# Optimization experiments

Hardware: AMD Instinct MI355X
Metric: run time of the kernel (lower is better)

## Reference

```python
import jax, jax.numpy as jnp
import numpy as np

D_MODEL = 1024
NUM_HEADS = 16
HEAD_DIM = D_MODEL // NUM_HEADS
HIDDEN = 4096
EPS = 1e-10


def _layernorm(x, gamma, beta):
    mean = jnp.mean(x, axis=-1, keepdims=True)
    var = jnp.var(x, axis=-1, keepdims=True)  # unbiased=False
    return gamma * (x - mean) / jnp.sqrt(var + EPS) + beta


def setup_inputs() -> dict:
    key = jax.random.key(0)
    ks = jax.random.split(key, 16)
    s = 0.02
    d, h = D_MODEL, HIDDEN
    inp = {
        "x": jax.random.normal(ks[0], (4, 2048, d), dtype=jnp.float32),
        "Wq": jax.random.normal(ks[1], (d, d), dtype=jnp.float32) * s,
        "bq": jnp.zeros((d,), jnp.float32),
        "Wk": jax.random.normal(ks[2], (d, d), dtype=jnp.float32) * s,
        "bk": jnp.zeros((d,), jnp.float32),
        "Wv": jax.random.normal(ks[3], (d, d), dtype=jnp.float32) * s,
        "bv": jnp.zeros((d,), jnp.float32),
        "Wo": jax.random.normal(ks[4], (d, d), dtype=jnp.float32) * s,
        "bo": jnp.zeros((d,), jnp.float32),
        "W1": jax.random.normal(ks[5], (d, h), dtype=jnp.float32) * s,
        "b1": jnp.zeros((h,), jnp.float32),
        "W2": jax.random.normal(ks[6], (h, d), dtype=jnp.float32) * s,
        "b2": jnp.zeros((d,), jnp.float32),
        "gamma1": jnp.ones((d,), jnp.float32),
        "beta1": jnp.zeros((d,), jnp.float32),
        "gamma2": jnp.ones((d,), jnp.float32),
        "beta2": jnp.zeros((d,), jnp.float32),
    }
    return inp


def reference(x, Wq, bq, Wk, bk, Wv, bv, Wo, bo, W1, b1, W2, b2,
              gamma1, beta1, gamma2, beta2):
    B, S, D = x.shape
    H, hd = NUM_HEADS, HEAD_DIM
    scale = jnp.sqrt(jnp.float32(hd))

    # --- sublayer 1: self-attention on norm(x), residual add ---
    xn = _layernorm(x, gamma1, beta1)
    Q = (xn @ Wq + bq).reshape(B, S, H, hd).transpose(0, 2, 1, 3)  # [B,H,S,hd]
    K = (xn @ Wk + bk).reshape(B, S, H, hd).transpose(0, 2, 1, 3)
    V = (xn @ Wv + bv).reshape(B, S, H, hd).transpose(0, 2, 1, 3)
    scores = jnp.einsum("bhqd,bhkd->bhqk", Q, K) / scale  # [B,H,S,S]
    attn = jax.nn.softmax(scores, axis=-1)
    ctx = jnp.einsum("bhqk,bhkd->bhqd", attn, V)  # [B,H,S,hd]
    ctx = ctx.transpose(0, 2, 1, 3).reshape(B, S, D)
    x = x + (ctx @ Wo + bo)

    # --- sublayer 2: FFN on norm(x), residual add ---
    xn = _layernorm(x, gamma2, beta2)
    h = jax.nn.gelu(xn @ W1 + b1, approximate=False)  # torch F.gelu default = erf
    x = x + (h @ W2 + b2)
    return x
```

## Files before the change

kernel.cpp:

```cpp
#include <hip/hip_runtime.h>
#include <stdint.h>

#define D_MODEL 1024
#define HIDDEN  4096
#define SEQ     2048
#define NTOK    8192
#define NHEAD   16
#define HDIM    64

typedef unsigned short u16;
typedef __attribute__((ext_vector_type(8))) __bf16 bf16x8;
typedef __attribute__((ext_vector_type(4))) float f32x4;

__device__ __forceinline__ u16 f2bf(float f) {
  union { float f; unsigned u; } c; c.f = f;
  unsigned u = c.u + 0x7fffu + ((c.u >> 16) & 1u);
  return (u16)(u >> 16);
}

__device__ __forceinline__ void gload16(const void* g, void* l) {
  __builtin_amdgcn_global_load_lds((const __attribute__((address_space(1))) void*)g,
                                   (__attribute__((address_space(3))) void*)l, 16, 0, 0);
}

__global__ void transpose_cvt4(const float* __restrict__ A0, const float* __restrict__ A1,
                               const float* __restrict__ A2, const float* __restrict__ A3,
                               u16* __restrict__ O) {
  __shared__ float t[32][33];
  const int z = blockIdx.z;
  const float* W = (z == 0) ? A0 : (z == 1) ? A1 : (z == 2) ? A2 : A3;
  u16* Wt = O + ((size_t)z << 20);
  const int k0 = blockIdx.y * 32, n0 = blockIdx.x * 32;
  const int tx = threadIdx.x, ty = threadIdx.y;
#pragma unroll
  for (int p = 0; p < 4; ++p)
    t[ty + p * 8][tx] = W[(size_t)(k0 + ty + p * 8) * D_MODEL + n0 + tx];
  __syncthreads();
#pragma unroll
  for (int p = 0; p < 4; ++p) {
    const int n = ty + p * 8;
    Wt[(size_t)(n0 + n) * D_MODEL + k0 + tx] = f2bf(t[tx][n]);
  }
}

__global__ void transpose_cvt(const float* __restrict__ W, u16* __restrict__ Wt, int K, int N) {
  __shared__ float t[32][33];
  const int k0 = blockIdx.y * 32, n0 = blockIdx.x * 32;
  const int tx = threadIdx.x, ty = threadIdx.y;
#pragma unroll
  for (int p = 0; p < 4; ++p)
    t[ty + p * 8][tx] = W[(size_t)(k0 + ty + p * 8) * N + n0 + tx];
  __syncthreads();
#pragma unroll
  for (int p = 0; p < 4; ++p) {
    const int n = ty + p * 8;
    Wt[(size_t)(n0 + n) * K + k0 + tx] = f2bf(t[tx][n]);
  }
}

__global__ __launch_bounds__(256)
void ln_kernel(const float* __restrict__ x, const float* __restrict__ gamma,
               const float* __restrict__ beta, u16* __restrict__ out) {
  const int row = blockIdx.x;
  const int tid = threadIdx.x;
  const float4 v = ((const float4*)(x + (size_t)row * D_MODEL))[tid];
  float s = v.x + v.y + v.z + v.w;
  float q = v.x * v.x + v.y * v.y + v.z * v.z + v.w * v.w;
#pragma unroll
  for (int o = 32; o > 0; o >>= 1) { s += __shfl_down(s, o); q += __shfl_down(q, o); }
  __shared__ float ps[4], pq[4];
  const int wid = tid >> 6, lane = tid & 63;
  if (lane == 0) { ps[wid] = s; pq[wid] = q; }
  __syncthreads();
  s = ps[0] + ps[1] + ps[2] + ps[3];
  q = pq[0] + pq[1] + pq[2] + pq[3];
  const float mean = s * (1.0f / D_MODEL);
  const float var = q * (1.0f / D_MODEL) - mean * mean;
  const float rstd = rsqrtf(var + 1e-10f);
  const float4 gv = ((const float4*)gamma)[tid];
  const float4 bv = ((const float4*)beta)[tid];
  ushort4 o4;
  o4.x = f2bf((v.x - mean) * rstd * gv.x + bv.x);
  o4.y = f2bf((v.y - mean) * rstd * gv.y + bv.y);
  o4.z = f2bf((v.z - mean) * rstd * gv.z + bv.z);
  o4.w = f2bf((v.w - mean) * rstd * gv.w + bv.w);
  ((ushort4*)(out + (size_t)row * D_MODEL))[tid] = o4;
}

#define SLOT_AE (256 * 32)
#define SLOT_BE (128 * 32)
#define SLOT_E  (SLOT_AE + SLOT_BE)
#define SLOT_BYTES (SLOT_E * 2)

template <int EPI, int KPY, int KPX>
__global__ __launch_bounds__(512, 4)
void gemm32(const u16* __restrict__ A, const u16* __restrict__ Bt,
            const float* __restrict__ bias, const float* __restrict__ bias2,
            const float* __restrict__ res, void* __restrict__ outp, void* __restrict__ outp2,
            int M, int N, int K) {
  __shared__ u16 Ls[3 * SLOT_E];
  const int tid = threadIdx.x;
  const int wid = tid >> 6, lane = tid & 63;
  const int g = lane >> 4, lr = lane & 15;
  const int wr = wid >> 1, wc = wid & 1;

  const int xcd = blockIdx.x & 7, l = blockIdx.x >> 3;
  int bx, by;
  if (KPY > 0) { by = xcd * KPY + (l % KPY); bx = l / KPY; }
  else         { bx = xcd * KPX + (l % KPX); by = l / KPX; }
  const int m0 = by * 256, n0 = bx * 128;

  const int NT = K >> 5;

  const int rA0 = tid >> 2, cc0 = ((tid & 3) ^ (rA0 & 3)) << 3;
  const int u1 = tid + 512;
  const int rA1 = u1 >> 2, cc1 = (((u1 & 3) ^ (rA1 & 3))) << 3;
  const u16* pA0 = A + (size_t)(m0 + rA0) * K + cc0;
  const u16* pA1 = A + (size_t)(m0 + rA1) * K + cc1;
  const u16* pB0 = Bt + (size_t)(n0 + rA0) * K + cc0;
  const int dA0 = wid * 1024;
  const int dA1 = wid * 1024 + 8192;
  const int dB0 = SLOT_AE * 2 + wid * 1024;

  auto stage = [&](int slot) {
    char* sb = (char*)Ls + slot * SLOT_BYTES;
    gload16(pA0, sb + dA0);
    gload16(pA1, sb + dA1);
    gload16(pB0, sb + dB0);
    pA0 += 32; pA1 += 32; pB0 += 32;
  };

  stage(0); stage(1); stage(2);

  f32x4 acc[4][4] = {};
  const int cx = (g ^ (lr & 3)) << 3;

  for (int t = 0; t < NT; ++t) {
    if (t + 3 <= NT)      asm volatile("s_waitcnt vmcnt(6)" ::: "memory");
    else if (t + 2 <= NT) asm volatile("s_waitcnt vmcnt(3)" ::: "memory");
    else                  asm volatile("s_waitcnt vmcnt(0)" ::: "memory");
    asm volatile("s_barrier" ::: "memory");

    const int slot = t % 3;
    const u16* sA = Ls + slot * SLOT_E;
    const u16* sB = sA + SLOT_AE;
    bf16x8 af[4], bfr[4];
#pragma unroll
    for (int mf = 0; mf < 4; ++mf)
      af[mf] = *(const bf16x8*)(sA + (wr * 64 + mf * 16 + lr) * 32 + cx);
#pragma unroll
    for (int nf = 0; nf < 4; ++nf)
      bfr[nf] = *(const bf16x8*)(sB + (wc * 64 + nf * 16 + lr) * 32 + cx);

    __builtin_amdgcn_s_setprio(1);
#pragma unroll
    for (int mf = 0; mf < 4; ++mf)
#pragma unroll
      for (int nf = 0; nf < 4; ++nf)
        acc[mf][nf] = __builtin_amdgcn_mfma_f32_16x16x32_bf16(af[mf], bfr[nf], acc[mf][nf], 0, 0, 0);
    __builtin_amdgcn_s_setprio(0);

    if (t + 3 < NT) {
      asm volatile("s_barrier" ::: "memory");
      stage(slot);
    }
  }

#pragma unroll
  for (int mf = 0; mf < 4; ++mf)
#pragma unroll
    for (int nf = 0; nf < 4; ++nf) {
      const int gn = n0 + wc * 64 + nf * 16 + lr;
      const int gm = m0 + wr * 64 + mf * 16 + 4 * g;
#pragma unroll
      for (int r = 0; r < 4; ++r) {
        const float av = acc[mf][nf][r];
        if (EPI == 0) {
          ((u16*)outp)[(size_t)(gm + r) * N + gn] = f2bf(av + bias[gn]);
        } else if (EPI == 1) {
          const size_t idx = (size_t)(gm + r) * N + gn;
          ((float*)outp)[idx] = av + bias[gn] + res[idx];
        } else if (EPI == 2) {
          const float v = av + bias[gn];
          ((u16*)outp)[(size_t)(gm + r) * N + gn] =
              f2bf(0.5f * v * (1.0f + erff(v * 0.7071067811865475f)));
        } else if (EPI == 3) {
          const int gn_p = (gn & ~63) | ((gn & 15) << 2) | ((gn >> 4) & 3);
          ((u16*)outp)[(size_t)(gm + r) * N + gn_p] = f2bf(av + bias[gm + r]);
        } else {
          const int side = gn >> 10, col = gn & 1023;
          u16* o = (u16*)(side ? outp2 : outp);
          float t_ = av + (side ? bias2[col] : bias[col]);
          if (!side) t_ *= 0.18033688011112042f;
          o[(size_t)(gm + r) * 1024 + col] = f2bf(t_);
        }
      }
    }
}

__global__ __launch_bounds__(256, 4)
void attn_kernel(const u16* __restrict__ Q, const u16* __restrict__ K,
                 const u16* __restrict__ Vt, u16* __restrict__ ctxo) {
  const int L = blockIdx.x;
  const int q0 = ((L >> 3) & 15) * 128;
  const int bh = ((L >> 7) << 3) | (L & 7);
  const int b = bh >> 4, h = bh & 15;
  const int tid = threadIdx.x, wid = tid >> 6, lane = tid & 63;
  const int g = lane >> 4, lr = lane & 15;
  const size_t base = ((size_t)b * SEQ) * D_MODEL + h * HDIM;
  const size_t vbase = ((size_t)h * HDIM) * NTOK + (size_t)b * SEQ;

#define AST 76
  __shared__ u16 Ks[64 * AST];
  __shared__ u16 Vts[64 * AST];
  __shared__ u16 Ps[128 * AST];

  const int qw = wid * 32;

#pragma unroll
  for (int i = 0; i < 4; ++i) {
    const int ch = tid + 256 * i, row = ch >> 3, j = ch & 7;
    *(bf16x8*)(Ps + row * AST + j * 8) =
        *(const bf16x8*)(Q + base + (size_t)(q0 + row) * D_MODEL + j * 8);
  }
  __syncthreads();
  bf16x8 aq[2][2];
#pragma unroll
  for (int qf = 0; qf < 2; ++qf)
#pragma unroll
    for (int ks = 0; ks < 2; ++ks)
      aq[qf][ks] = *(const bf16x8*)(Ps + (qw + qf * 16 + lr) * AST + ks * 32 + g * 8);

  f32x4 o[2][4] = {};
  float lrun[2][4] = {};

  for (int kv0 = 0; kv0 < SEQ; kv0 += 64) {
    __syncthreads();
#pragma unroll
    for (int i = 0; i < 2; ++i) {
      const int row = (tid >> 3) + i * 32, j = tid & 7;
      *(bf16x8*)(Ks + row * AST + j * 8) =
          *(const bf16x8*)(K + base + (size_t)(kv0 + row) * D_MODEL + j * 8);
      *(bf16x8*)(Vts + row * AST + j * 8) =
          *(const bf16x8*)(Vt + vbase + (size_t)row * NTOK + kv0 + j * 8);
    }
    __syncthreads();

    f32x4 s[2][4] = {};
    __builtin_amdgcn_s_setprio(1);
#pragma unroll
    for (int ks = 0; ks < 2; ++ks)
#pragma unroll
      for (int kf = 0; kf < 4; ++kf) {
        const bf16x8 bk = *(const bf16x8*)(Ks + (kf * 16 + lr) * AST + ks * 32 + g * 8);
#pragma unroll
        for (int qf = 0; qf < 2; ++qf)
          s[qf][kf] = __builtin_amdgcn_mfma_f32_16x16x32_bf16(aq[qf][ks], bk, s[qf][kf], 0, 0, 0);
      }
    __builtin_amdgcn_s_setprio(0);

#pragma unroll
    for (int qf = 0; qf < 2; ++qf)
#pragma unroll
      for (int r = 0; r < 4; ++r) {
        float p0, p1, p2, p3;
        asm("v_exp_f32 %0, %1" : "=v"(p0) : "v"(s[qf][0][r]));
        asm("v_exp_f32 %0, %1" : "=v"(p1) : "v"(s[qf][1][r]));
        asm("v_exp_f32 %0, %1" : "=v"(p2) : "v"(s[qf][2][r]));
        asm("v_exp_f32 %0, %1" : "=v"(p3) : "v"(s[qf][3][r]));
        lrun[qf][r] += (p0 + p1) + (p2 + p3);
        unsigned lo, hi;
        asm("v_cvt_pk_bf16_f32 %0, %1, %2" : "=v"(lo) : "v"(p0), "v"(p1));
        asm("v_cvt_pk_bf16_f32 %0, %1, %2" : "=v"(hi) : "v"(p2), "v"(p3));
        *(uint2*)(Ps + (qw + qf * 16 + 4 * g + r) * AST + lr * 4) = make_uint2(lo, hi);
      }
    asm volatile("s_waitcnt lgkmcnt(0)" ::: "memory");

    __builtin_amdgcn_s_setprio(1);
#pragma unroll
    for (int ks = 0; ks < 2; ++ks) {
      bf16x8 pf[2];
#pragma unroll
      for (int qf = 0; qf < 2; ++qf)
        pf[qf] = *(const bf16x8*)(Ps + (qw + qf * 16 + lr) * AST + ks * 32 + g * 8);
#pragma unroll
      for (int df = 0; df < 4; ++df) {
        const bf16x8 vf = *(const bf16x8*)(Vts + (df * 16 + lr) * AST + ks * 32 + g * 8);
#pragma unroll
        for (int qf = 0; qf < 2; ++qf)
          o[qf][df] = __builtin_amdgcn_mfma_f32_16x16x32_bf16(pf[qf], vf, o[qf][df], 0, 0, 0);
      }
    }
    __builtin_amdgcn_s_setprio(0);
  }

#pragma unroll
  for (int off = 1; off < 16; off <<= 1)
#pragma unroll
    for (int qf = 0; qf < 2; ++qf)
#pragma unroll
      for (int r = 0; r < 4; ++r)
        lrun[qf][r] += __shfl_xor(lrun[qf][r], off);

#pragma unroll
  for (int qf = 0; qf < 2; ++qf)
#pragma unroll
    for (int r = 0; r < 4; ++r) {
      const float rinv = 1.0f / lrun[qf][r];
      const int qrow = q0 + qw + qf * 16 + 4 * g + r;
#pragma unroll
      for (int df = 0; df < 4; ++df)
        ctxo[base + (size_t)qrow * D_MODEL + df * 16 + lr] = f2bf(o[qf][df][r] * rinv);
    }
#undef AST
}

extern "C" void kernel_launch(void* const* d_in, const int* in_sizes, int n_in,
                              void* d_out, int out_size, void* d_ws, size_t ws_size,
                              hipStream_t stream) {
  const float* x  = (const float*)d_in[0];
  const float* Wq = (const float*)d_in[1];
  const float* bq = (const float*)d_in[2];
  const float* Wk = (const float*)d_in[3];
  const float* bk = (const float*)d_in[4];
  const float* Wv = (const float*)d_in[5];
  const float* bv = (const float*)d_in[6];
  const float* Wo = (const float*)d_in[7];
  const float* bo = (const float*)d_in[8];
  const float* W1 = (const float*)d_in[9];
  const float* b1 = (const float*)d_in[10];
  const float* W2 = (const float*)d_in[11];
  const float* b2 = (const float*)d_in[12];
  const float* gamma1 = (const float*)d_in[13];
  const float* beta1  = (const float*)d_in[14];
  const float* gamma2 = (const float*)d_in[15];
  const float* beta2  = (const float*)d_in[16];
  float* out = (float*)d_out;

  const size_t M1 = 1u << 20;
  u16* w   = (u16*)d_ws;
  u16* WtQ = w;
  u16* WtV = w + 2 * M1;
  u16* WtO = w + 3 * M1;
  u16* Wt1 = w + 4 * M1;
  u16* Wt2 = w + 8 * M1;
  u16* xn  = w + 12 * M1;
  u16* Qb  = w + 20 * M1;
  u16* Kb  = w + 28 * M1;
  u16* Vtb = w + 36 * M1;
  u16* ctx = w + 44 * M1;
  u16* hb  = w + 20 * M1;
  float* x1 = (float*)(w + 52 * M1);

  const dim3 tb(32, 8);
  transpose_cvt4<<<dim3(32, 32, 4), tb, 0, stream>>>(Wq, Wk, Wv, Wo, WtQ);
  transpose_cvt<<<dim3(HIDDEN / 32, D_MODEL / 32), tb, 0, stream>>>(W1, Wt1, D_MODEL, HIDDEN);
  transpose_cvt<<<dim3(D_MODEL / 32, HIDDEN / 32), tb, 0, stream>>>(W2, Wt2, HIDDEN, D_MODEL);

  ln_kernel<<<NTOK, 256, 0, stream>>>(x, gamma1, beta1, xn);

  gemm32<6, 4, 0><<<512, 512, 0, stream>>>(xn, WtQ, bq, bk, nullptr, Qb, Kb,
                                           NTOK, 2048, D_MODEL);
  gemm32<3, 0, 8><<<256, 512, 0, stream>>>(WtV, xn, bv, nullptr, nullptr, Vtb, nullptr,
                                           D_MODEL, NTOK, D_MODEL);

  attn_kernel<<<1024, 256, 0, stream>>>(Qb, Kb, Vtb, ctx);

  gemm32<1, 4, 0><<<256, 512, 0, stream>>>(ctx, WtO, bo, nullptr, x, x1, nullptr,
                                           NTOK, D_MODEL, D_MODEL);

  ln_kernel<<<NTOK, 256, 0, stream>>>(x1, gamma2, beta2, xn);

  gemm32<2, 4, 0><<<1024, 512, 0, stream>>>(xn, Wt1, b1, nullptr, nullptr, hb, nullptr,
                                            NTOK, HIDDEN, D_MODEL);
  gemm32<1, 4, 0><<<256, 512, 0, stream>>>(hb, Wt2, b2, nullptr, x1, out, nullptr,
                                           NTOK, D_MODEL, HIDDEN);
}
```

Baseline: 384.6 us.

## Replace triple-buffered 256x128 GEMM with single-buffered 128x128 tile kernel

Replaces the 512-thread GEMM, which used a 256x128 tile and a three-slot async LDS pipeline with vmcnt-based waits, with a 256-thread 128x128 tile kernel. The new kernel uses a single LDS buffer with two barriers per K-step and no prefetch overlap. Grid sizes and block-swizzle parameters are adjusted to match. This doubles the block count and shrinks LDS use per block, but global loads are no longer overlapped with MFMA work, and A/B reuse per tile drops.

```diff
diff --git a/kernel.cpp b/kernel.cpp
--- a/kernel.cpp
+++ b/kernel.cpp
@@ -87,71 +87,53 @@
   ((ushort4*)(out + (size_t)row * D_MODEL))[tid] = o4;
 }
 
-#define SLOT_AE (256 * 32)
-#define SLOT_BE (128 * 32)
-#define SLOT_E  (SLOT_AE + SLOT_BE)
-#define SLOT_BYTES (SLOT_E * 2)
-
 template <int EPI, int KPY, int KPX>
-__global__ __launch_bounds__(512, 4)
-void gemm32(const u16* __restrict__ A, const u16* __restrict__ Bt,
+__global__ __launch_bounds__(256, 3)
+void gemm97(const u16* __restrict__ A, const u16* __restrict__ Bt,
             const float* __restrict__ bias, const float* __restrict__ bias2,
             const float* __restrict__ res, void* __restrict__ outp, void* __restrict__ outp2,
             int M, int N, int K) {
-  __shared__ u16 Ls[3 * SLOT_E];
+  __shared__ u16 As[128 * 32];
+  __shared__ u16 Bs[128 * 32];
   const int tid = threadIdx.x;
   const int wid = tid >> 6, lane = tid & 63;
   const int g = lane >> 4, lr = lane & 15;
-  const int wr = wid >> 1, wc = wid & 1;
+  const int wm = (wid & 1) << 6, wn = (wid >> 1) << 6;
 
   const int xcd = blockIdx.x & 7, l = blockIdx.x >> 3;
   int bx, by;
   if (KPY > 0) { by = xcd * KPY + (l % KPY); bx = l / KPY; }
   else         { bx = xcd * KPX + (l % KPX); by = l / KPX; }
-  const int m0 = by * 256, n0 = bx * 128;
+  const int m0 = by * 128, n0 = bx * 128;
 
   const int NT = K >> 5;
 
-  const int rA0 = tid >> 2, cc0 = ((tid & 3) ^ (rA0 & 3)) << 3;
-  const int u1 = tid + 512;
-  const int rA1 = u1 >> 2, cc1 = (((u1 & 3) ^ (rA1 & 3))) << 3;
-  const u16* pA0 = A + (size_t)(m0 + rA0) * K + cc0;
-  const u16* pA1 = A + (size_t)(m0 + rA1) * K + cc1;
-  const u16* pB0 = Bt + (size_t)(n0 + rA0) * K + cc0;
-  const int dA0 = wid * 1024;
-  const int dA1 = wid * 1024 + 8192;
-  const int dB0 = SLOT_AE * 2 + wid * 1024;
-
-  auto stage = [&](int slot) {
-    char* sb = (char*)Ls + slot * SLOT_BYTES;
-    gload16(pA0, sb + dA0);
-    gload16(pA1, sb + dA1);
-    gload16(pB0, sb + dB0);
-    pA0 += 32; pA1 += 32; pB0 += 32;
-  };
-
-  stage(0); stage(1); stage(2);
+  const int r0 = tid >> 2;
+  const int c0 = ((tid & 3) ^ (r0 & 3)) << 3;
+  const u16* pA0 = A + (size_t)(m0 + r0) * K + c0;
+  const u16* pA1 = A + (size_t)(m0 + r0 + 64) * K + c0;
+  const u16* pB0 = Bt + (size_t)(n0 + r0) * K + c0;
+  const u16* pB1 = Bt + (size_t)(n0 + r0 + 64) * K + c0;
+  const int d0 = (tid & 192) * 16;
 
   f32x4 acc[4][4] = {};
   const int cx = (g ^ (lr & 3)) << 3;
 
   for (int t = 0; t < NT; ++t) {
-    if (t + 3 <= NT)      asm volatile("s_waitcnt vmcnt(6)" ::: "memory");
-    else if (t + 2 <= NT) asm volatile("s_waitcnt vmcnt(3)" ::: "memory");
-    else                  asm volatile("s_waitcnt vmcnt(0)" ::: "memory");
-    asm volatile("s_barrier" ::: "memory");
-
-    const int slot = t % 3;
-    const u16* sA = Ls + slot * SLOT_E;
-    const u16* sB = sA + SLOT_AE;
+    __syncthreads();
+    gload16(pA0, (char*)As + d0);
+    gload16(pA1, (char*)As + d0 + 4096);
+    gload16(pB0, (char*)Bs + d0);
+    gload16(pB1, (char*)Bs + d0 + 4096);
+    pA0 += 32; pA1 += 32; pB0 += 32; pB1 += 32;
+    __syncthreads();
+
     bf16x8 af[4], bfr[4];
 #pragma unroll
-    for (int mf = 0; mf < 4; ++mf)
-      af[mf] = *(const bf16x8*)(sA + (wr * 64 + mf * 16 + lr) * 32 + cx);
-#pragma unroll
-    for (int nf = 0; nf < 4; ++nf)
-      bfr[nf] = *(const bf16x8*)(sB + (wc * 64 + nf * 16 + lr) * 32 + cx);
-
+    for (int f = 0; f < 4; ++f) {
+      af[f] = *(const bf16x8*)(As + (wm + f * 16 + lr) * 32 + cx);
+      bfr[f] = *(const bf16x8*)(Bs + (wn + f * 16 + lr) * 32 + cx);
+    }
     __builtin_amdgcn_s_setprio(1);
 #pragma unroll
     for (int mf = 0; mf < 4; ++mf)
@@ -159,19 +141,14 @@
       for (int nf = 0; nf < 4; ++nf)
         acc[mf][nf] = __builtin_amdgcn_mfma_f32_16x16x32_bf16(af[mf], bfr[nf], acc[mf][nf], 0, 0, 0);
     __builtin_amdgcn_s_setprio(0);
-
-    if (t + 3 < NT) {
-      asm volatile("s_barrier" ::: "memory");
-      stage(slot);
-    }
   }
 
 #pragma unroll
   for (int mf = 0; mf < 4; ++mf)
 #pragma unroll
     for (int nf = 0; nf < 4; ++nf) {
-      const int gn = n0 + wc * 64 + nf * 16 + lr;
-      const int gm = m0 + wr * 64 + mf * 16 + 4 * g;
+      const int gn = n0 + wn + nf * 16 + lr;
+      const int gm = m0 + wm + mf * 16 + 4 * g;
 #pragma unroll
       for (int r = 0; r < 4; ++r) {
         const float av = acc[mf][nf][r];
@@ -359,20 +336,20 @@
 
   ln_kernel<<<NTOK, 256, 0, stream>>>(x, gamma1, beta1, xn);
 
-  gemm32<6, 4, 0><<<512, 512, 0, stream>>>(xn, WtQ, bq, bk, nullptr, Qb, Kb,
-                                           NTOK, 2048, D_MODEL);
-  gemm32<3, 0, 8><<<256, 512, 0, stream>>>(WtV, xn, bv, nullptr, nullptr, Vtb, nullptr,
+  gemm97<6, 8, 0><<<1024, 256, 0, stream>>>(xn, WtQ, bq, bk, nullptr, Qb, Kb,
+                                            NTOK, 2048, D_MODEL);
+  gemm97<3, 1, 0><<<512, 256, 0, stream>>>(WtV, xn, bv, nullptr, nullptr, Vtb, nullptr,
                                            D_MODEL, NTOK, D_MODEL);
 
   attn_kernel<<<1024, 256, 0, stream>>>(Qb, Kb, Vtb, ctx);
 
-  gemm32<1, 4, 0><<<256, 512, 0, stream>>>(ctx, WtO, bo, nullptr, x, x1, nullptr,
+  gemm97<1, 8, 0><<<512, 256, 0, stream>>>(ctx, WtO, bo, nullptr, x, x1, nullptr,
                                            NTOK, D_MODEL, D_MODEL);
 
   ln_kernel<<<NTOK, 256, 0, stream>>>(x1, gamma2, beta2, xn);
 
-  gemm32<2, 4, 0><<<1024, 512, 0, stream>>>(xn, Wt1, b1, nullptr, nullptr, hb, nullptr,
+  gemm97<2, 8, 0><<<2048, 256, 0, stream>>>(xn, Wt1, b1, nullptr, nullptr, hb, nullptr,
                                             NTOK, HIDDEN, D_MODEL);
-  gemm32<1, 4, 0><<<256, 512, 0, stream>>>(hb, Wt2, b2, nullptr, x1, out, nullptr,
+  gemm97<1, 8, 0><<<512, 256, 0, stream>>>(hb, Wt2, b2, nullptr, x1, out, nullptr,
                                            NTOK, D_MODEL, HIDDEN);
 }
```

After: 398.7 us. 3.7% more time.

## Add 128x128-tile GEMM with 64-wide K steps for FFN layers

Applied to the files above, without the earlier changes.

Adds a new gemm64 kernel that uses 128x128 output tiles, 256 threads, 64-element K slices with XOR-swizzled LDS, and 4x4 MFMA fragments per wave. The two FFN GEMMs now use it in place of the prior gemm32 kernel, with more, smaller blocks and a different XCD mapping. The aim is to raise block-level parallelism and occupancy and cut per-iteration sync overhead by doing more MFMA work per barrier. The loop is single-buffered with two barriers per K step, so memory latency may not be hidden as well as in the old kernel.

```diff
diff --git a/kernel.cpp b/kernel.cpp
--- a/kernel.cpp
+++ b/kernel.cpp
@@ -198,6 +198,104 @@
     }
 }
 
+template <int EPI, int KPY, int KPX>
+__global__ __launch_bounds__(256, 3)
+void gemm64(const u16* __restrict__ A, const u16* __restrict__ Bt,
+            const float* __restrict__ bias, const float* __restrict__ bias2,
+            const float* __restrict__ res, void* __restrict__ outp, void* __restrict__ outp2,
+            int M, int N, int K) {
+  __shared__ u16 As[128 * 64];
+  __shared__ u16 Bs[128 * 64];
+  const int tid = threadIdx.x;
+  const int wid = tid >> 6, lane = tid & 63;
+  const int g = lane >> 4, lr = lane & 15;
+  const int wm = (wid & 1) << 6, wn = (wid >> 1) << 6;
+
+  const int xcd = blockIdx.x & 7, l = blockIdx.x >> 3;
+  int bx, by;
+  if (KPY > 0) { by = xcd * KPY + (l % KPY); bx = l / KPY; }
+  else         { bx = xcd * KPX + (l % KPX); by = l / KPX; }
+  const int m0 = by * 128, n0 = bx * 128;
+
+  const int NT = K >> 6;
+
+  const int r0 = tid >> 3;
+  const int csw = ((tid & 7) ^ (r0 & 7)) << 3;
+  const u16* pA[4];
+  const u16* pB[4];
+#pragma unroll
+  for (int i = 0; i < 4; ++i) {
+    pA[i] = A + (size_t)(m0 + r0 + i * 32) * K + csw;
+    pB[i] = Bt + (size_t)(n0 + r0 + i * 32) * K + csw;
+  }
+  const int db = (tid & 192) * 16;
+
+  f32x4 acc[4][4] = {};
+
+  for (int t = 0; t < NT; ++t) {
+    __syncthreads();
+#pragma unroll
+    for (int i = 0; i < 4; ++i) {
+      gload16(pA[i], (char*)As + db + i * 4096);
+      gload16(pB[i], (char*)Bs + db + i * 4096);
+      pA[i] += 64; pB[i] += 64;
+    }
+    __syncthreads();
+
+#pragma unroll
+    for (int ks = 0; ks < 2; ++ks) {
+      bf16x8 af[4], bfr[4];
+#pragma unroll
+      for (int f = 0; f < 4; ++f) {
+        const int ra = wm + f * 16 + lr;
+        const int rb = wn + f * 16 + lr;
+        const int co = ((ks * 4 + g) ^ (lr & 7)) * 8;
+        af[f] = *(const bf16x8*)(As + ra * 64 + co);
+        bfr[f] = *(const bf16x8*)(Bs + rb * 64 + co);
+      }
+      __builtin_amdgcn_s_setprio(1);
+#pragma unroll
+      for (int mf = 0; mf < 4; ++mf)
+#pragma unroll
+        for (int nf = 0; nf < 4; ++nf)
+          acc[mf][nf] =
+              __builtin_amdgcn_mfma_f32_16x16x32_bf16(af[mf], bfr[nf], acc[mf][nf], 0, 0, 0);
+      __builtin_amdgcn_s_setprio(0);
+    }
+  }
+
+#pragma unroll
+  for (int mf = 0; mf < 4; ++mf)
+#pragma unroll
+    for (int nf = 0; nf < 4; ++nf) {
+      const int gn = n0 + wn + nf * 16 + lr;
+      const int gm = m0 + wm + mf * 16 + 4 * g;
+#pragma unroll
+      for (int r = 0; r < 4; ++r) {
+        const float av = acc[mf][nf][r];
+        if (EPI == 0) {
+          ((u16*)outp)[(size_t)(gm + r) * N + gn] = f2bf(av + bias[gn]);
+        } else if (EPI == 1) {
+          const size_t idx = (size_t)(gm + r) * N + gn;
+          ((float*)outp)[idx] = av + bias[gn] + res[idx];
+        } else if (EPI == 2) {
+          const float v = av + bias[gn];
+          ((u16*)outp)[(size_t)(gm + r) * N + gn] =
+              f2bf(0.5f * v * (1.0f + erff(v * 0.7071067811865475f)));
+        } else if (EPI == 3) {
+          const int gn_p = (gn & ~63) | ((gn & 15) << 2) | ((gn >> 4) & 3);
+          ((u16*)outp)[(size_t)(gm + r) * N + gn_p] = f2bf(av + bias[gm + r]);
+        } else {
+          const int side = gn >> 10, col = gn & 1023;
+          u16* o = (u16*)(side ? outp2 : outp);
+          float t_ = av + (side ? bias2[col] : bias[col]);
+          if (!side) t_ *= 0.18033688011112042f;
+          o[(size_t)(gm + r) * 1024 + col] = f2bf(t_);
+        }
+      }
+    }
+}
+
 __global__ __launch_bounds__(256, 4)
 void attn_kernel(const u16* __restrict__ Q, const u16* __restrict__ K,
                  const u16* __restrict__ Vt, u16* __restrict__ ctxo) {
@@ -371,8 +469,8 @@
 
   ln_kernel<<<NTOK, 256, 0, stream>>>(x1, gamma2, beta2, xn);
 
-  gemm32<2, 4, 0><<<1024, 512, 0, stream>>>(xn, Wt1, b1, nullptr, nullptr, hb, nullptr,
+  gemm64<2, 8, 0><<<2048, 256, 0, stream>>>(xn, Wt1, b1, nullptr, nullptr, hb, nullptr,
                                             NTOK, HIDDEN, D_MODEL);
-  gemm32<1, 4, 0><<<256, 512, 0, stream>>>(hb, Wt2, b2, nullptr, x1, out, nullptr,
+  gemm64<1, 8, 0><<<512, 256, 0, stream>>>(hb, Wt2, b2, nullptr, x1, out, nullptr,
                                            NTOK, D_MODEL, HIDDEN);
 }
```

New measurement: 363.9 us. 5.4% less time.
